# Kernel optimization log

Hardware: AMD Instinct MI355X
Metric: run time of the kernel (lower is better)

## Reference

```python
import jax, jax.numpy as jnp
import numpy as np

EMBED_DIM = 1024
NUM_HEADS = 16
HEAD_DIM = EMBED_DIM // NUM_HEADS


def setup_inputs() -> dict:
    key = jax.random.key(0)
    ks = jax.random.split(key, 5)
    scale = 1.0 / np.sqrt(EMBED_DIM)
    x = jax.random.normal(ks[0], (2, 2048, EMBED_DIM), dtype=jnp.float32)
    W_qkv = jax.random.uniform(ks[1], (EMBED_DIM, 3 * EMBED_DIM), jnp.float32, -scale, scale)
    b_qkv = jax.random.uniform(ks[2], (3 * EMBED_DIM,), jnp.float32, -scale, scale)
    W_out = jax.random.uniform(ks[3], (EMBED_DIM, EMBED_DIM), jnp.float32, -scale, scale)
    b_out = jax.random.uniform(ks[4], (EMBED_DIM,), jnp.float32, -scale, scale)
    return {"x": x, "W_qkv": W_qkv, "b_qkv": b_qkv, "W_out": W_out, "b_out": b_out}


def reference(x, W_qkv, b_qkv, W_out, b_out):
    B, T, C = x.shape
    H, D = NUM_HEADS, HEAD_DIM
    qkv = x @ W_qkv + b_qkv                       # [B,T,3C]
    q, k, v = jnp.split(qkv, 3, axis=-1)
    # [B,T,C] -> [B,H,T,D]
    q = q.reshape(B, T, H, D).transpose(0, 2, 1, 3)
    k = k.reshape(B, T, H, D).transpose(0, 2, 1, 3)
    v = v.reshape(B, T, H, D).transpose(0, 2, 1, 3)
    scores = jnp.einsum('bhqd,bhkd->bhqk', q, k) / np.sqrt(D)
    attn = jax.nn.softmax(scores, axis=-1)
    out = jnp.einsum('bhqk,bhkd->bhqd', attn, v)  # [B,H,T,D]
    out = out.transpose(0, 2, 1, 3).reshape(B, T, C)
    return out @ W_out + b_out
```

## Files before the change

kernel.cpp:

```cpp
#include <hip/hip_runtime.h>
#include <hip/hip_bf16.h>

#define TB 2048
#define CC 1024
#define HH 16
#define DD 64
#define MM 4096
#define N3 3072
#define KVB 128
#define NT (TB / KVB)

typedef __bf16 bf16x8 __attribute__((ext_vector_type(8)));
typedef float f32x4 __attribute__((ext_vector_type(4)));
typedef unsigned short ushort8 __attribute__((ext_vector_type(8)));
typedef unsigned short u16;

#define QSCALE 0.180336880693612f

__device__ __forceinline__ u16 f2b(float f) {
    unsigned int x = __float_as_uint(f);
    x = (x + 0x7fffu + ((x >> 16) & 1u)) >> 16;
    return (u16)x;
}

__device__ __forceinline__ unsigned cvt_pk_bf16(float lo, float hi) {
    unsigned r;
    asm("v_cvt_pk_bf16_f32 %0, %1, %2" : "=v"(r) : "v"(lo), "v"(hi));
    return r;
}

__device__ __forceinline__ void gld16(const u16* g, u16* l) {
    __builtin_amdgcn_global_load_lds(
        (const __attribute__((address_space(1))) unsigned int*)g,
        (__attribute__((address_space(3))) unsigned int*)l, 16, 0, 0);
}

__global__ __launch_bounds__(256) void prep(const float* __restrict__ x,
                                            u16* __restrict__ xb,
                                            const float* __restrict__ wqkv,
                                            u16* __restrict__ wqkvT,
                                            const float* __restrict__ wout,
                                            u16* __restrict__ woutT) {
    __shared__ float tl[64][65];
    const int bx = blockIdx.x;
    const int tid = threadIdx.x;
    if (bx < 4096) {
        int i = (bx * 256 + tid) * 4;
        float4 v = *reinterpret_cast<const float4*>(x + i);
        union { u16 u[4]; uint2 v2; } r;
        r.u[0] = f2b(v.x); r.u[1] = f2b(v.y); r.u[2] = f2b(v.z); r.u[3] = f2b(v.w);
        *reinterpret_cast<uint2*>(xb + i) = r.v2;
        return;
    }
    const int idx = bx - 4096;
    const int nb = idx & 63, kb = idx >> 6;
    const float* in; u16* out; int N, n0;
    if (nb < 48) { in = wqkv; out = wqkvT; N = 3072; n0 = nb * 64; }
    else         { in = wout; out = woutT; N = 1024; n0 = (nb - 48) * 64; }
    const int k0 = kb * 64;
#pragma unroll
    for (int rep = 0; rep < 16; ++rep) {
        int id2 = rep * 256 + tid;
        int r = id2 >> 6, c = id2 & 63;
        tl[r][c] = in[(size_t)(k0 + r) * N + n0 + c];
    }
    __syncthreads();
#pragma unroll
    for (int rep = 0; rep < 16; ++rep) {
        int id2 = rep * 256 + tid;
        int r = id2 >> 6, c = id2 & 63;
        out[(size_t)(n0 + r) * 1024 + k0 + c] = f2b(tl[c][r]);
    }
}

__global__ __launch_bounds__(256) void gemm_qkv(const u16* __restrict__ xb,
                                                const u16* __restrict__ wT,
                                                const float* __restrict__ bias,
                                                u16* __restrict__ qg,
                                                u16* __restrict__ kg,
                                                u16* __restrict__ vtg) {
    __shared__ u16 smem[2 * 128 * 64];
    u16* As = smem;
    u16* Bs = smem + 128 * 64;
    const int m0 = blockIdx.y * 128, n0 = blockIdx.x * 128;
    const int tid = threadIdx.x;
    const int w = tid >> 6, lane = tid & 63, lr = lane & 15, h = lane >> 4;
    const int wr = w >> 1, wc = w & 1;
    f32x4 acc[4][4] = {};

    for (int k0 = 0; k0 < 1024; k0 += 64) {
        __syncthreads();
#pragma unroll
        for (int j = 0; j < 4; ++j) {
            int L = j * 256 + tid;
            int r = L >> 3, c = L & 7;
            int csw = (c ^ (r & 7)) << 3;
            gld16(xb + (size_t)(m0 + r) * 1024 + k0 + csw, As + L * 8);
            gld16(wT + (size_t)(n0 + r) * 1024 + k0 + csw, Bs + L * 8);
        }
        __syncthreads();
#pragma unroll
        for (int kk = 0; kk < 2; ++kk) {
            bf16x8 a[4], b[4];
            int cc = kk * 4 + h;
#pragma unroll
            for (int m = 0; m < 4; ++m) {
                int R = wr * 64 + m * 16 + lr;
                a[m] = *reinterpret_cast<const bf16x8*>((const char*)As + R * 128 + ((cc ^ (R & 7)) << 4));
            }
#pragma unroll
            for (int n = 0; n < 4; ++n) {
                int R = wc * 64 + n * 16 + lr;
                b[n] = *reinterpret_cast<const bf16x8*>((const char*)Bs + R * 128 + ((cc ^ (R & 7)) << 4));
            }
#pragma unroll
            for (int m = 0; m < 4; ++m)
#pragma unroll
                for (int n = 0; n < 4; ++n)
                    acc[m][n] = __builtin_amdgcn_mfma_f32_16x16x32_bf16(a[m], b[n], acc[m][n], 0, 0, 0);
        }
    }

    const int nthird = n0 >> 10;
    const int b = m0 >> 11, t0 = m0 & 2047;
    if (nthird == 2) {
        __syncthreads();
#pragma unroll
        for (int n = 0; n < 4; ++n) {
            int nloc = wc * 64 + n * 16 + lr;
            unsigned xorv = (unsigned)(nloc & 15) << 4;
            float bv = bias[n0 + nloc];
#pragma unroll
            for (int m = 0; m < 4; ++m) {
                int mloc = wr * 64 + m * 16 + h * 4;
                int mp = (mloc & ~31) | (((mloc >> 2) & 3) << 3) | (((mloc >> 4) & 1) << 2);
                union { u16 u[4]; unsigned long long ll; } pk4;
#pragma unroll
                for (int reg = 0; reg < 4; ++reg)
                    pk4.u[reg] = f2b(acc[m][n][reg] + bv);
                *reinterpret_cast<unsigned long long*>(
                    (char*)smem + nloc * 256 + ((unsigned)(mp * 2) ^ xorv)) = pk4.ll;
            }
        }
        __syncthreads();
        const int c16 = tid & 15;
#pragma unroll
        for (int step = 0; step < 8; ++step) {
            int row = (tid >> 4) + step * 16;
            ushort8 vch = *reinterpret_cast<const ushort8*>(
                (const char*)smem + row * 256 + ((unsigned)((c16 ^ (row & 15)) << 4)));
            int c1 = (n0 + row) & 1023;
            int hh = c1 >> 6, dd = c1 & 63;
            *reinterpret_cast<ushort8*>(
                vtg + ((size_t)(b * HH + hh) * DD + dd) * TB + t0 + c16 * 8) = vch;
        }
    } else {
        const float qs = (nthird == 0) ? QSCALE : 1.0f;
        __syncthreads();
#pragma unroll
        for (int n = 0; n < 4; ++n) {
            int nloc = wc * 64 + n * 16 + lr;
            float bv = bias[n0 + nloc];
#pragma unroll
            for (int m = 0; m < 4; ++m) {
#pragma unroll
                for (int reg = 0; reg < 4; ++reg) {
                    int mloc = wr * 64 + m * 16 + h * 4 + reg;
                    *reinterpret_cast<u16*>((char*)smem + mloc * 256 +
                        ((unsigned)(nloc * 2) ^ ((unsigned)(mloc & 15) << 4)))
                        = f2b((acc[m][n][reg] + bv) * qs);
                }
            }
        }
        __syncthreads();
        u16* dst = (nthird == 0) ? qg : kg;
        const int c16 = tid & 15;
#pragma unroll
        for (int step = 0; step < 8; ++step) {
            int row = (tid >> 4) + step * 16;
            ushort8 vch = *reinterpret_cast<const ushort8*>(
                (const char*)smem + row * 256 + ((unsigned)((c16 ^ (row & 15)) << 4)));
            int colbase = c16 * 8;
            int c1 = (n0 + colbase) & 1023;
            int hh = c1 >> 6, dd = c1 & 63;
            *reinterpret_cast<ushort8*>(
                dst + ((size_t)(b * HH + hh) * TB + (t0 + row)) * DD + dd) = vch;
        }
    }
}

__global__ __launch_bounds__(512, 4) void attn(const u16* __restrict__ qg,
                                               const u16* __restrict__ kg,
                                               const u16* __restrict__ vtg,
                                               u16* __restrict__ ao) {
    __shared__ u16 Kt[2][KVB * 64];
    __shared__ u16 Vt[2][64 * KVB];
    const int bh = blockIdx.x;
    const int q0 = blockIdx.y * 128;
    const int tid = threadIdx.x, w = tid >> 6, lane = tid & 63;
    const int lr = lane & 15, h = lane >> 4;
    const u16* qb = qg + (size_t)bh * TB * DD;
    const u16* kb = kg + (size_t)bh * TB * DD;
    const u16* vb = vtg + (size_t)bh * DD * TB;

#define STAGE(buf, kp, vp) do {                                                         \
    _Pragma("unroll")                                                                   \
    for (int j = 0; j < 2; ++j) {                                                       \
        int L = j * 512 + tid;                                                          \
        int rk = L >> 3, ck = L & 7;                                                    \
        gld16((kp) + (size_t)rk * DD + ((ck ^ (rk & 7)) << 3), Kt[buf] + L * 8);        \
        int rv = L >> 4, cv = L & 15;                                                   \
        gld16((vp) + (size_t)rv * TB + ((cv ^ (rv & 15)) << 3), Vt[buf] + L * 8);       \
    } } while (0)

    bf16x8 bq[2];
#pragma unroll
    for (int kk = 0; kk < 2; ++kk)
        bq[kk] = *reinterpret_cast<const bf16x8*>(qb + (size_t)(q0 + w * 16 + lr) * DD + kk * 32 + h * 8);

    f32x4 o[4] = {};
    float m_r = -1e30f;
    float l_r = 0.f;
    const f32x4 zero4 = {0.f, 0.f, 0.f, 0.f};

    auto tile_body = [&](const u16* ktc, const u16* vtc) {
        f32x4 s[8];
        __builtin_amdgcn_s_setprio(1);
        {
            int cc0 = h;
#pragma unroll
            for (int ng = 0; ng < 8; ++ng) {
                int R = ng * 16 + lr;
                bf16x8 ak = *reinterpret_cast<const bf16x8*>((const char*)ktc + R * 128 + ((cc0 ^ (R & 7)) << 4));
                s[ng] = __builtin_amdgcn_mfma_f32_16x16x32_bf16(ak, bq[0], zero4, 0, 0, 0);
            }
            int cc1 = 4 + h;
#pragma unroll
            for (int ng = 0; ng < 8; ++ng) {
                int R = ng * 16 + lr;
                bf16x8 ak = *reinterpret_cast<const bf16x8*>((const char*)ktc + R * 128 + ((cc1 ^ (R & 7)) << 4));
                s[ng] = __builtin_amdgcn_mfma_f32_16x16x32_bf16(ak, bq[1], s[ng], 0, 0, 0);
            }
        }
        __builtin_amdgcn_s_setprio(0);

        float tmx[8];
#pragma unroll
        for (int ng = 0; ng < 8; ++ng)
            tmx[ng] = fmaxf(fmaxf(s[ng][0], s[ng][1]), fmaxf(s[ng][2], s[ng][3]));
        float pm = fmaxf(fmaxf(fmaxf(tmx[0], tmx[1]), fmaxf(tmx[2], tmx[3])),
                         fmaxf(fmaxf(tmx[4], tmx[5]), fmaxf(tmx[6], tmx[7])));
        pm = fmaxf(pm, __shfl_xor(pm, 16));
        pm = fmaxf(pm, __shfl_xor(pm, 32));

        if (!__all(pm - m_r <= 8.0f)) {
            float mn = fmaxf(m_r, pm);
            float fr = __builtin_amdgcn_exp2f(m_r - mn);
            m_r = mn;
            l_r *= fr;
#pragma unroll
            for (int reg = 0; reg < 4; ++reg) {
                float fro = __shfl(fr, h * 4 + reg);
#pragma unroll
                for (int ngd = 0; ngd < 4; ++ngd)
                    o[ngd][reg] *= fro;
            }
        }

        float ps[8];
#pragma unroll
        for (int ng = 0; ng < 8; ++ng) {
            s[ng][0] = __builtin_amdgcn_exp2f(s[ng][0] - m_r);
            s[ng][1] = __builtin_amdgcn_exp2f(s[ng][1] - m_r);
            s[ng][2] = __builtin_amdgcn_exp2f(s[ng][2] - m_r);
            s[ng][3] = __builtin_amdgcn_exp2f(s[ng][3] - m_r);
            ps[ng] = (s[ng][0] + s[ng][1]) + (s[ng][2] + s[ng][3]);
        }
        float sum = ((ps[0] + ps[1]) + (ps[2] + ps[3])) + ((ps[4] + ps[5]) + (ps[6] + ps[7]));
        sum += __shfl_xor(sum, 16);
        sum += __shfl_xor(sum, 32);
        l_r += sum;

        __builtin_amdgcn_s_setprio(1);
#pragma unroll
        for (int kk = 0; kk < 4; ++kk) {
            union { unsigned u[4]; bf16x8 v; } ap;
            ap.u[0] = cvt_pk_bf16(s[2 * kk][0], s[2 * kk][1]);
            ap.u[1] = cvt_pk_bf16(s[2 * kk][2], s[2 * kk][3]);
            ap.u[2] = cvt_pk_bf16(s[2 * kk + 1][0], s[2 * kk + 1][1]);
            ap.u[3] = cvt_pk_bf16(s[2 * kk + 1][2], s[2 * kk + 1][3]);
            int cpos = kk * 4 + h;
#pragma unroll
            for (int ngd = 0; ngd < 4; ++ngd) {
                int d = ngd * 16 + lr;
                bf16x8 bv = *reinterpret_cast<const bf16x8*>((const char*)vtc + d * 256 + ((cpos ^ (d & 15)) << 4));
                o[ngd] = __builtin_amdgcn_mfma_f32_16x16x32_bf16(ap.v, bv, o[ngd], 0, 0, 0);
            }
        }
        __builtin_amdgcn_s_setprio(0);
    };

    STAGE(0, kb, vb);
    const u16* kp = kb + KVB * DD;
    const u16* vp = vb + KVB;
    __syncthreads();

#pragma unroll 1
    for (int kt2 = 0; kt2 < NT / 2; ++kt2) {
        STAGE(1, kp, vp);
        kp += KVB * DD; vp += KVB;
        tile_body(Kt[0], Vt[0]);
        __syncthreads();
        if (kt2 < NT / 2 - 1) {
            STAGE(0, kp, vp);
            kp += KVB * DD; vp += KVB;
        }
        tile_body(Kt[1], Vt[1]);
        __syncthreads();
    }
#undef STAGE

    float linv[4];
#pragma unroll
    for (int reg = 0; reg < 4; ++reg)
        linv[reg] = 1.0f / __shfl(l_r, h * 4 + reg);

    const int b = bh >> 4, hh = bh & 15;
#pragma unroll
    for (int ngd = 0; ngd < 4; ++ngd) {
#pragma unroll
        for (int reg = 0; reg < 4; ++reg) {
            int t = q0 + w * 16 + h * 4 + reg;
            int col = hh * DD + ngd * 16 + lr;
            ao[((size_t)(b * TB + t)) * CC + col] = f2b(o[ngd][reg] * linv[reg]);
        }
    }
}

__global__ __launch_bounds__(256) void gemm_out(const u16* __restrict__ ao,
                                                const u16* __restrict__ wT,
                                                const float* __restrict__ bias,
                                                float* __restrict__ out) {
    __shared__ u16 As[64 * 64];
    __shared__ u16 Bs[128 * 64];
    const int m0 = blockIdx.y * 64, n0 = blockIdx.x * 128;
    const int tid = threadIdx.x;
    const int w = tid >> 6, lane = tid & 63, lr = lane & 15, h = lane >> 4;
    f32x4 acc[4][2] = {};

    for (int k0 = 0; k0 < 1024; k0 += 64) {
        __syncthreads();
#pragma unroll
        for (int j = 0; j < 2; ++j) {
            int L = j * 256 + tid;
            int r = L >> 3, c = L & 7;
            gld16(ao + (size_t)(m0 + r) * 1024 + k0 + ((c ^ (r & 7)) << 3), As + L * 8);
        }
#pragma unroll
        for (int j = 0; j < 4; ++j) {
            int L = j * 256 + tid;
            int r = L >> 3, c = L & 7;
            gld16(wT + (size_t)(n0 + r) * 1024 + k0 + ((c ^ (r & 7)) << 3), Bs + L * 8);
        }
        __syncthreads();
#pragma unroll
        for (int kk = 0; kk < 2; ++kk) {
            bf16x8 a[4], b[2];
            int cc = kk * 4 + h;
#pragma unroll
            for (int m = 0; m < 4; ++m) {
                int R = m * 16 + lr;
                a[m] = *reinterpret_cast<const bf16x8*>((const char*)As + R * 128 + ((cc ^ (R & 7)) << 4));
            }
#pragma unroll
            for (int n = 0; n < 2; ++n) {
                int R = w * 32 + n * 16 + lr;
                b[n] = *reinterpret_cast<const bf16x8*>((const char*)Bs + R * 128 + ((cc ^ (R & 7)) << 4));
            }
#pragma unroll
            for (int m = 0; m < 4; ++m)
#pragma unroll
                for (int n = 0; n < 2; ++n)
                    acc[m][n] = __builtin_amdgcn_mfma_f32_16x16x32_bf16(a[m], b[n], acc[m][n], 0, 0, 0);
        }
    }

#pragma unroll
    for (int n = 0; n < 2; ++n) {
        int ng = n0 + w * 32 + n * 16 + lr;
        float bv = bias[ng];
#pragma unroll
        for (int m = 0; m < 4; ++m) {
#pragma unroll
            for (int reg = 0; reg < 4; ++reg) {
                int mg = m0 + m * 16 + h * 4 + reg;
                out[(size_t)mg * 1024 + ng] = acc[m][n][reg] + bv;
            }
        }
    }
}

extern "C" void kernel_launch(void* const* d_in, const int* in_sizes, int n_in,
                              void* d_out, int out_size, void* d_ws, size_t ws_size,
                              hipStream_t stream) {
    const float* x     = (const float*)d_in[0];
    const float* W_qkv = (const float*)d_in[1];
    const float* b_qkv = (const float*)d_in[2];
    const float* W_out = (const float*)d_in[3];
    const float* b_out = (const float*)d_in[4];
    float* out = (float*)d_out;

    char* ws = (char*)d_ws;
    u16* xb    = (u16*)(ws);
    u16* wqkvT = (u16*)(ws + (size_t)( 8u << 20));
    u16* woutT = (u16*)(ws + (size_t)(14u << 20));
    u16* qg    = (u16*)(ws + (size_t)(16u << 20));
    u16* kg    = (u16*)(ws + (size_t)(24u << 20));
    u16* vtg   = (u16*)(ws + (size_t)(32u << 20));
    u16* ao    = xb;

    hipLaunchKernelGGL(prep, dim3(5120), dim3(256), 0, stream, x, xb, W_qkv, wqkvT, W_out, woutT);
    hipLaunchKernelGGL(gemm_qkv, dim3(24, 32), dim3(256), 0, stream, xb, wqkvT, b_qkv, qg, kg, vtg);
    hipLaunchKernelGGL(attn, dim3(32, 16), dim3(512), 0, stream, qg, kg, vtg, ao);
    hipLaunchKernelGGL(gemm_out, dim3(8, 64), dim3(256), 0, stream, ao, woutT, b_out, out);
}
```

Baseline: 118.4 us.

## Software-pipeline attention: overlap next tile's QK^T with current softmax and PV

```diff
diff --git a/kernel.cpp b/kernel.cpp
--- a/kernel.cpp
+++ b/kernel.cpp
@@ -203,15 +203,98 @@
     const u16* kb = kg + (size_t)bh * TB * DD;
     const u16* vb = vtg + (size_t)bh * DD * TB;
 
-#define STAGE(buf, kp, vp) do {                                                         \
+#define STAGE_K(buf, kt) do {                                                           \
     _Pragma("unroll")                                                                   \
     for (int j = 0; j < 2; ++j) {                                                       \
         int L = j * 512 + tid;                                                          \
         int rk = L >> 3, ck = L & 7;                                                    \
-        gld16((kp) + (size_t)rk * DD + ((ck ^ (rk & 7)) << 3), Kt[buf] + L * 8);        \
+        gld16(kb + (size_t)((kt) * KVB + rk) * DD + ((ck ^ (rk & 7)) << 3),             \
+              Kt[buf] + L * 8);                                                         \
+    } } while (0)
+#define STAGE_V(buf, kt) do {                                                           \
+    _Pragma("unroll")                                                                   \
+    for (int j = 0; j < 2; ++j) {                                                       \
+        int L = j * 512 + tid;                                                          \
         int rv = L >> 4, cv = L & 15;                                                   \
-        gld16((vp) + (size_t)rv * TB + ((cv ^ (rv & 15)) << 3), Vt[buf] + L * 8);       \
+        gld16(vb + (size_t)rv * TB + (kt) * KVB + ((cv ^ (rv & 15)) << 3),              \
+              Vt[buf] + L * 8);                                                         \
     } } while (0)
+
+#define QK_PHASE(S, KBUF) do {                                                          \
+    __builtin_amdgcn_s_setprio(1);                                                      \
+    const u16* ktc_ = Kt[KBUF];                                                         \
+    _Pragma("unroll")                                                                   \
+    for (int ng = 0; ng < 8; ++ng) {                                                    \
+        int R = ng * 16 + lr;                                                           \
+        bf16x8 ak = *reinterpret_cast<const bf16x8*>(                                   \
+            (const char*)ktc_ + R * 128 + (((h) ^ (R & 7)) << 4));                      \
+        S[ng] = __builtin_amdgcn_mfma_f32_16x16x32_bf16(ak, bq[0], zero4, 0, 0, 0);     \
+    }                                                                                   \
+    _Pragma("unroll")                                                                   \
+    for (int ng = 0; ng < 8; ++ng) {                                                    \
+        int R = ng * 16 + lr;                                                           \
+        bf16x8 ak = *reinterpret_cast<const bf16x8*>(                                   \
+            (const char*)ktc_ + R * 128 + (((4 + h) ^ (R & 7)) << 4));                  \
+        S[ng] = __builtin_amdgcn_mfma_f32_16x16x32_bf16(ak, bq[1], S[ng], 0, 0, 0);     \
+    }                                                                                   \
+    __builtin_amdgcn_s_setprio(0);                                                      \
+} while (0)
+
+#define SMPV(S, VBUF) do {                                                              \
+    const u16* vtc_ = Vt[VBUF];                                                         \
+    float tmx[8];                                                                       \
+    _Pragma("unroll")                                                                   \
+    for (int ng = 0; ng < 8; ++ng)                                                      \
+        tmx[ng] = fmaxf(fmaxf(S[ng][0], S[ng][1]), fmaxf(S[ng][2], S[ng][3]));          \
+    float pm = fmaxf(fmaxf(fmaxf(tmx[0], tmx[1]), fmaxf(tmx[2], tmx[3])),               \
+                     fmaxf(fmaxf(tmx[4], tmx[5]), fmaxf(tmx[6], tmx[7])));              \
+    pm = fmaxf(pm, __shfl_xor(pm, 16));                                                 \
+    pm = fmaxf(pm, __shfl_xor(pm, 32));                                                 \
+    if (!__all(pm - m_r <= 8.0f)) {                                                     \
+        float mn = fmaxf(m_r, pm);                                                      \
+        float fr = __builtin_amdgcn_exp2f(m_r - mn);                                    \
+        m_r = mn;                                                                       \
+        l_r *= fr;                                                                      \
+        _Pragma("unroll")                                                               \
+        for (int reg = 0; reg < 4; ++reg) {                                             \
+            float fro = __shfl(fr, h * 4 + reg);                                        \
+            _Pragma("unroll")                                                           \
+            for (int ngd = 0; ngd < 4; ++ngd)                                           \
+                o[ngd][reg] *= fro;                                                     \
+        }                                                                               \
+    }                                                                                   \
+    float ps[8];                                                                        \
+    _Pragma("unroll")                                                                   \
+    for (int ng = 0; ng < 8; ++ng) {                                                    \
+        S[ng][0] = __builtin_amdgcn_exp2f(S[ng][0] - m_r);                              \
+        S[ng][1] = __builtin_amdgcn_exp2f(S[ng][1] - m_r);                              \
+        S[ng][2] = __builtin_amdgcn_exp2f(S[ng][2] - m_r);                              \
+        S[ng][3] = __builtin_amdgcn_exp2f(S[ng][3] - m_r);                              \
+        ps[ng] = (S[ng][0] + S[ng][1]) + (S[ng][2] + S[ng][3]);                         \
+    }                                                                                   \
+    float sum = ((ps[0] + ps[1]) + (ps[2] + ps[3])) + ((ps[4] + ps[5]) + (ps[6] + ps[7])); \
+    sum += __shfl_xor(sum, 16);                                                         \
+    sum += __shfl_xor(sum, 32);                                                         \
+    l_r += sum;                                                                         \
+    __builtin_amdgcn_s_setprio(1);                                                      \
+    _Pragma("unroll")                                                                   \
+    for (int kk = 0; kk < 4; ++kk) {                                                    \
+        union { unsigned u[4]; bf16x8 v; } ap;                                          \
+        ap.u[0] = cvt_pk_bf16(S[2 * kk][0], S[2 * kk][1]);                              \
+        ap.u[1] = cvt_pk_bf16(S[2 * kk][2], S[2 * kk][3]);                              \
+        ap.u[2] = cvt_pk_bf16(S[2 * kk + 1][0], S[2 * kk + 1][1]);                      \
+        ap.u[3] = cvt_pk_bf16(S[2 * kk + 1][2], S[2 * kk + 1][3]);                      \
+        int cpos = kk * 4 + h;                                                          \
+        _Pragma("unroll")                                                               \
+        for (int ngd = 0; ngd < 4; ++ngd) {                                             \
+            int d = ngd * 16 + lr;                                                      \
+            bf16x8 bv = *reinterpret_cast<const bf16x8*>(                               \
+                (const char*)vtc_ + d * 256 + ((cpos ^ (d & 15)) << 4));                \
+            o[ngd] = __builtin_amdgcn_mfma_f32_16x16x32_bf16(ap.v, bv, o[ngd], 0, 0, 0);\
+        }                                                                               \
+    }                                                                                   \
+    __builtin_amdgcn_s_setprio(0);                                                      \
+} while (0)
 
     bf16x8 bq[2];
 #pragma unroll
@@ -222,103 +305,39 @@
     float m_r = -1e30f;
     float l_r = 0.f;
     const f32x4 zero4 = {0.f, 0.f, 0.f, 0.f};
-
-    auto tile_body = [&](const u16* ktc, const u16* vtc) {
-        f32x4 s[8];
-        __builtin_amdgcn_s_setprio(1);
-        {
-            int cc0 = h;
-#pragma unroll
-            for (int ng = 0; ng < 8; ++ng) {
-                int R = ng * 16 + lr;
-                bf16x8 ak = *reinterpret_cast<const bf16x8*>((const char*)ktc + R * 128 + ((cc0 ^ (R & 7)) << 4));
-                s[ng] = __builtin_amdgcn_mfma_f32_16x16x32_bf16(ak, bq[0], zero4, 0, 0, 0);
-            }
-            int cc1 = 4 + h;
-#pragma unroll
-            for (int ng = 0; ng < 8; ++ng) {
-                int R = ng * 16 + lr;
-                bf16x8 ak = *reinterpret_cast<const bf16x8*>((const char*)ktc + R * 128 + ((cc1 ^ (R & 7)) << 4));
-                s[ng] = __builtin_amdgcn_mfma_f32_16x16x32_bf16(ak, bq[1], s[ng], 0, 0, 0);
-            }
-        }
-        __builtin_amdgcn_s_setprio(0);
-
-        float tmx[8];
-#pragma unroll
-        for (int ng = 0; ng < 8; ++ng)
-            tmx[ng] = fmaxf(fmaxf(s[ng][0], s[ng][1]), fmaxf(s[ng][2], s[ng][3]));
-        float pm = fmaxf(fmaxf(fmaxf(tmx[0], tmx[1]), fmaxf(tmx[2], tmx[3])),
-                         fmaxf(fmaxf(tmx[4], tmx[5]), fmaxf(tmx[6], tmx[7])));
-        pm = fmaxf(pm, __shfl_xor(pm, 16));
-        pm = fmaxf(pm, __shfl_xor(pm, 32));
-
-        if (!__all(pm - m_r <= 8.0f)) {
-            float mn = fmaxf(m_r, pm);
-            float fr = __builtin_amdgcn_exp2f(m_r - mn);
-            m_r = mn;
-            l_r *= fr;
-#pragma unroll
-            for (int reg = 0; reg < 4; ++reg) {
-                float fro = __shfl(fr, h * 4 + reg);
-#pragma unroll
-                for (int ngd = 0; ngd < 4; ++ngd)
-                    o[ngd][reg] *= fro;
-            }
-        }
-
-        float ps[8];
-#pragma unroll
-        for (int ng = 0; ng < 8; ++ng) {
-            s[ng][0] = __builtin_amdgcn_exp2f(s[ng][0] - m_r);
-            s[ng][1] = __builtin_amdgcn_exp2f(s[ng][1] - m_r);
-            s[ng][2] = __builtin_amdgcn_exp2f(s[ng][2] - m_r);
-            s[ng][3] = __builtin_amdgcn_exp2f(s[ng][3] - m_r);
-            ps[ng] = (s[ng][0] + s[ng][1]) + (s[ng][2] + s[ng][3]);
-        }
-        float sum = ((ps[0] + ps[1]) + (ps[2] + ps[3])) + ((ps[4] + ps[5]) + (ps[6] + ps[7]));
-        sum += __shfl_xor(sum, 16);
-        sum += __shfl_xor(sum, 32);
-        l_r += sum;
-
-        __builtin_amdgcn_s_setprio(1);
-#pragma unroll
-        for (int kk = 0; kk < 4; ++kk) {
-            union { unsigned u[4]; bf16x8 v; } ap;
-            ap.u[0] = cvt_pk_bf16(s[2 * kk][0], s[2 * kk][1]);
-            ap.u[1] = cvt_pk_bf16(s[2 * kk][2], s[2 * kk][3]);
-            ap.u[2] = cvt_pk_bf16(s[2 * kk + 1][0], s[2 * kk + 1][1]);
-            ap.u[3] = cvt_pk_bf16(s[2 * kk + 1][2], s[2 * kk + 1][3]);
-            int cpos = kk * 4 + h;
-#pragma unroll
-            for (int ngd = 0; ngd < 4; ++ngd) {
-                int d = ngd * 16 + lr;
-                bf16x8 bv = *reinterpret_cast<const bf16x8*>((const char*)vtc + d * 256 + ((cpos ^ (d & 15)) << 4));
-                o[ngd] = __builtin_amdgcn_mfma_f32_16x16x32_bf16(ap.v, bv, o[ngd], 0, 0, 0);
-            }
-        }
-        __builtin_amdgcn_s_setprio(0);
-    };
-
-    STAGE(0, kb, vb);
-    const u16* kp = kb + KVB * DD;
-    const u16* vp = vb + KVB;
+    f32x4 sA[8], sB[8];
+
+    STAGE_K(0, 0);
+    STAGE_V(0, 0);
+    STAGE_K(1, 1);
     __syncthreads();
+    QK_PHASE(sA, 0);
+    __syncthreads();
 
 #pragma unroll 1
-    for (int kt2 = 0; kt2 < NT / 2; ++kt2) {
-        STAGE(1, kp, vp);
-        kp += KVB * DD; vp += KVB;
-        tile_body(Kt[0], Vt[0]);
-        __syncthreads();
-        if (kt2 < NT / 2 - 1) {
-            STAGE(0, kp, vp);
-            kp += KVB * DD; vp += KVB;
-        }
-        tile_body(Kt[1], Vt[1]);
-        __syncthreads();
-    }
-#undef STAGE
+    for (int u = 0; u < 7; ++u) {
+        const int t = 2 * u;
+        STAGE_V(1, t + 1);
+        STAGE_K(0, t + 2);
+        QK_PHASE(sB, 1);
+        SMPV(sA, 0);
+        __syncthreads();
+        STAGE_V(0, t + 2);
+        STAGE_K(1, t + 3);
+        QK_PHASE(sA, 0);
+        SMPV(sB, 1);
+        __syncthreads();
+    }
+    STAGE_V(1, 15);
+    QK_PHASE(sB, 1);
+    SMPV(sA, 0);
+    __syncthreads();
+    SMPV(sB, 1);
+
+#undef STAGE_K
+#undef STAGE_V
+#undef QK_PHASE
+#undef SMPV
 
     float linv[4];
 #pragma unroll
```

After: 129.1 us. 1.09x slower.

## Switch attention to 32x32x16 MFMA with 4 waves of 32 query rows

Applied to the files above, without the earlier changes.

```diff
diff --git a/kernel.cpp b/kernel.cpp
--- a/kernel.cpp
+++ b/kernel.cpp
@@ -12,6 +12,7 @@
 
 typedef __bf16 bf16x8 __attribute__((ext_vector_type(8)));
 typedef float f32x4 __attribute__((ext_vector_type(4)));
+typedef float f32x16 __attribute__((ext_vector_type(16)));
 typedef unsigned short ushort8 __attribute__((ext_vector_type(8)));
 typedef unsigned short u16;
 
@@ -133,7 +134,7 @@
 #pragma unroll
             for (int m = 0; m < 4; ++m) {
                 int mloc = wr * 64 + m * 16 + h * 4;
-                int mp = (mloc & ~31) | (((mloc >> 2) & 3) << 3) | (((mloc >> 4) & 1) << 2);
+                int mp = (mloc & ~15) | (mloc & 3) | ((mloc & 4) << 1) | ((mloc & 8) >> 1);
                 union { u16 u[4]; unsigned long long ll; } pk4;
 #pragma unroll
                 for (int reg = 0; reg < 4; ++reg)
@@ -189,7 +190,7 @@
     }
 }
 
-__global__ __launch_bounds__(512, 4) void attn(const u16* __restrict__ qg,
+__global__ __launch_bounds__(256, 2) void attn(const u16* __restrict__ qg,
                                                const u16* __restrict__ kg,
                                                const u16* __restrict__ vtg,
                                                u16* __restrict__ ao) {
@@ -198,59 +199,58 @@
     const int bh = blockIdx.x;
     const int q0 = blockIdx.y * 128;
     const int tid = threadIdx.x, w = tid >> 6, lane = tid & 63;
-    const int lr = lane & 15, h = lane >> 4;
+    const int ln = lane & 31, H = lane >> 5;
     const u16* qb = qg + (size_t)bh * TB * DD;
     const u16* kb = kg + (size_t)bh * TB * DD;
     const u16* vb = vtg + (size_t)bh * DD * TB;
 
 #define STAGE(buf, kp, vp) do {                                                         \
     _Pragma("unroll")                                                                   \
-    for (int j = 0; j < 2; ++j) {                                                       \
-        int L = j * 512 + tid;                                                          \
+    for (int j = 0; j < 4; ++j) {                                                       \
+        int L = j * 256 + tid;                                                          \
         int rk = L >> 3, ck = L & 7;                                                    \
         gld16((kp) + (size_t)rk * DD + ((ck ^ (rk & 7)) << 3), Kt[buf] + L * 8);        \
         int rv = L >> 4, cv = L & 15;                                                   \
         gld16((vp) + (size_t)rv * TB + ((cv ^ (rv & 15)) << 3), Vt[buf] + L * 8);       \
     } } while (0)
 
-    bf16x8 bq[2];
-#pragma unroll
-    for (int kk = 0; kk < 2; ++kk)
-        bq[kk] = *reinterpret_cast<const bf16x8*>(qb + (size_t)(q0 + w * 16 + lr) * DD + kk * 32 + h * 8);
-
-    f32x4 o[4] = {};
+    bf16x8 bq[4];
+#pragma unroll
+    for (int dc = 0; dc < 4; ++dc)
+        bq[dc] = *reinterpret_cast<const bf16x8*>(
+            qb + (size_t)(q0 + w * 32 + ln) * DD + dc * 16 + H * 8);
+
+    f32x16 o[2] = {};
     float m_r = -1e30f;
     float l_r = 0.f;
-    const f32x4 zero4 = {0.f, 0.f, 0.f, 0.f};
+    f32x16 zero16 = {};
 
     auto tile_body = [&](const u16* ktc, const u16* vtc) {
-        f32x4 s[8];
+        f32x16 s[4];
         __builtin_amdgcn_s_setprio(1);
-        {
-            int cc0 = h;
-#pragma unroll
-            for (int ng = 0; ng < 8; ++ng) {
-                int R = ng * 16 + lr;
-                bf16x8 ak = *reinterpret_cast<const bf16x8*>((const char*)ktc + R * 128 + ((cc0 ^ (R & 7)) << 4));
-                s[ng] = __builtin_amdgcn_mfma_f32_16x16x32_bf16(ak, bq[0], zero4, 0, 0, 0);
-            }
-            int cc1 = 4 + h;
-#pragma unroll
-            for (int ng = 0; ng < 8; ++ng) {
-                int R = ng * 16 + lr;
-                bf16x8 ak = *reinterpret_cast<const bf16x8*>((const char*)ktc + R * 128 + ((cc1 ^ (R & 7)) << 4));
-                s[ng] = __builtin_amdgcn_mfma_f32_16x16x32_bf16(ak, bq[1], s[ng], 0, 0, 0);
+#pragma unroll
+        for (int kb4 = 0; kb4 < 4; ++kb4) {
+            int R = kb4 * 32 + ln;
+            const char* krow = (const char*)ktc + R * 128;
+#pragma unroll
+            for (int dc = 0; dc < 4; ++dc) {
+                bf16x8 ak = *reinterpret_cast<const bf16x8*>(
+                    krow + (((dc * 2 + H) ^ (R & 7)) << 4));
+                s[kb4] = __builtin_amdgcn_mfma_f32_32x32x16_bf16(
+                    ak, bq[dc], dc == 0 ? zero16 : s[kb4], 0, 0, 0);
             }
         }
         __builtin_amdgcn_s_setprio(0);
 
-        float tmx[8];
-#pragma unroll
-        for (int ng = 0; ng < 8; ++ng)
-            tmx[ng] = fmaxf(fmaxf(s[ng][0], s[ng][1]), fmaxf(s[ng][2], s[ng][3]));
-        float pm = fmaxf(fmaxf(fmaxf(tmx[0], tmx[1]), fmaxf(tmx[2], tmx[3])),
-                         fmaxf(fmaxf(tmx[4], tmx[5]), fmaxf(tmx[6], tmx[7])));
-        pm = fmaxf(pm, __shfl_xor(pm, 16));
+        float pm = s[0][0];
+#pragma unroll
+        for (int kb4 = 0; kb4 < 4; ++kb4) {
+            float t0 = fmaxf(fmaxf(s[kb4][0], s[kb4][1]), fmaxf(s[kb4][2], s[kb4][3]));
+            float t1 = fmaxf(fmaxf(s[kb4][4], s[kb4][5]), fmaxf(s[kb4][6], s[kb4][7]));
+            float t2 = fmaxf(fmaxf(s[kb4][8], s[kb4][9]), fmaxf(s[kb4][10], s[kb4][11]));
+            float t3 = fmaxf(fmaxf(s[kb4][12], s[kb4][13]), fmaxf(s[kb4][14], s[kb4][15]));
+            pm = fmaxf(pm, fmaxf(fmaxf(t0, t1), fmaxf(t2, t3)));
+        }
         pm = fmaxf(pm, __shfl_xor(pm, 32));
 
         if (!__all(pm - m_r <= 8.0f)) {
@@ -259,42 +259,44 @@
             m_r = mn;
             l_r *= fr;
 #pragma unroll
-            for (int reg = 0; reg < 4; ++reg) {
-                float fro = __shfl(fr, h * 4 + reg);
-#pragma unroll
-                for (int ngd = 0; ngd < 4; ++ngd)
-                    o[ngd][reg] *= fro;
-            }
-        }
-
-        float ps[8];
-#pragma unroll
-        for (int ng = 0; ng < 8; ++ng) {
-            s[ng][0] = __builtin_amdgcn_exp2f(s[ng][0] - m_r);
-            s[ng][1] = __builtin_amdgcn_exp2f(s[ng][1] - m_r);
-            s[ng][2] = __builtin_amdgcn_exp2f(s[ng][2] - m_r);
-            s[ng][3] = __builtin_amdgcn_exp2f(s[ng][3] - m_r);
-            ps[ng] = (s[ng][0] + s[ng][1]) + (s[ng][2] + s[ng][3]);
-        }
-        float sum = ((ps[0] + ps[1]) + (ps[2] + ps[3])) + ((ps[4] + ps[5]) + (ps[6] + ps[7]));
-        sum += __shfl_xor(sum, 16);
+            for (int ngd = 0; ngd < 2; ++ngd)
+#pragma unroll
+                for (int r = 0; r < 16; ++r)
+                    o[ngd][r] *= fr;
+        }
+
+        float sum = 0.f;
+#pragma unroll
+        for (int kb4 = 0; kb4 < 4; ++kb4) {
+            float ps = 0.f;
+#pragma unroll
+            for (int r = 0; r < 16; ++r) {
+                s[kb4][r] = __builtin_amdgcn_exp2f(s[kb4][r] - m_r);
+                ps += s[kb4][r];
+            }
+            sum += ps;
+        }
         sum += __shfl_xor(sum, 32);
         l_r += sum;
 
         __builtin_amdgcn_s_setprio(1);
 #pragma unroll
-        for (int kk = 0; kk < 4; ++kk) {
-            union { unsigned u[4]; bf16x8 v; } ap;
-            ap.u[0] = cvt_pk_bf16(s[2 * kk][0], s[2 * kk][1]);
-            ap.u[1] = cvt_pk_bf16(s[2 * kk][2], s[2 * kk][3]);
-            ap.u[2] = cvt_pk_bf16(s[2 * kk + 1][0], s[2 * kk + 1][1]);
-            ap.u[3] = cvt_pk_bf16(s[2 * kk + 1][2], s[2 * kk + 1][3]);
-            int cpos = kk * 4 + h;
-#pragma unroll
-            for (int ngd = 0; ngd < 4; ++ngd) {
-                int d = ngd * 16 + lr;
-                bf16x8 bv = *reinterpret_cast<const bf16x8*>((const char*)vtc + d * 256 + ((cpos ^ (d & 15)) << 4));
-                o[ngd] = __builtin_amdgcn_mfma_f32_16x16x32_bf16(ap.v, bv, o[ngd], 0, 0, 0);
+        for (int kb4 = 0; kb4 < 4; ++kb4) {
+#pragma unroll
+            for (int b1 = 0; b1 < 2; ++b1) {
+                union { unsigned u[4]; bf16x8 v; } ap;
+                ap.u[0] = cvt_pk_bf16(s[kb4][8 * b1 + 0], s[kb4][8 * b1 + 1]);
+                ap.u[1] = cvt_pk_bf16(s[kb4][8 * b1 + 2], s[kb4][8 * b1 + 3]);
+                ap.u[2] = cvt_pk_bf16(s[kb4][8 * b1 + 4], s[kb4][8 * b1 + 5]);
+                ap.u[3] = cvt_pk_bf16(s[kb4][8 * b1 + 6], s[kb4][8 * b1 + 7]);
+                int c = kb4 * 2 + b1;
+#pragma unroll
+                for (int ngd = 0; ngd < 2; ++ngd) {
+                    int d = ngd * 32 + ln;
+                    bf16x8 av = *reinterpret_cast<const bf16x8*>(
+                        (const char*)vtc + d * 256 + (((c * 2 + H) ^ (d & 15)) << 4));
+                    o[ngd] = __builtin_amdgcn_mfma_f32_32x32x16_bf16(av, ap.v, o[ngd], 0, 0, 0);
+                }
             }
         }
         __builtin_amdgcn_s_setprio(0);
@@ -320,19 +322,20 @@
     }
 #undef STAGE
 
-    float linv[4];
-#pragma unroll
-    for (int reg = 0; reg < 4; ++reg)
-        linv[reg] = 1.0f / __shfl(l_r, h * 4 + reg);
-
+    const float linv = 1.0f / l_r;
     const int b = bh >> 4, hh = bh & 15;
-#pragma unroll
-    for (int ngd = 0; ngd < 4; ++ngd) {
-#pragma unroll
-        for (int reg = 0; reg < 4; ++reg) {
-            int t = q0 + w * 16 + h * 4 + reg;
-            int col = hh * DD + ngd * 16 + lr;
-            ao[((size_t)(b * TB + t)) * CC + col] = f2b(o[ngd][reg] * linv[reg]);
+    const int q = q0 + w * 32 + ln;
+    u16* aorow = ao + (size_t)(b * TB + q) * CC + hh * 64;
+#pragma unroll
+    for (int ngd = 0; ngd < 2; ++ngd) {
+#pragma unroll
+        for (int rg = 0; rg < 4; ++rg) {
+            int dbase = ngd * 32 + 8 * rg + 4 * H;
+            union { u16 u[4]; unsigned long long ll; } pk;
+#pragma unroll
+            for (int r2 = 0; r2 < 4; ++r2)
+                pk.u[r2] = f2b(o[ngd][4 * rg + r2] * linv);
+            *reinterpret_cast<unsigned long long*>(aorow + dbase) = pk.ll;
         }
     }
 }
@@ -421,6 +424,6 @@
 
     hipLaunchKernelGGL(prep, dim3(5120), dim3(256), 0, stream, x, xb, W_qkv, wqkvT, W_out, woutT);
     hipLaunchKernelGGL(gemm_qkv, dim3(24, 32), dim3(256), 0, stream, xb, wqkvT, b_qkv, qg, kg, vtg);
-    hipLaunchKernelGGL(attn, dim3(32, 16), dim3(512), 0, stream, qg, kg, vtg, ao);
+    hipLaunchKernelGGL(attn, dim3(32, 16), dim3(256), 0, stream, qg, kg, vtg, ao);
     hipLaunchKernelGGL(gemm_out, dim3(8, 64), dim3(256), 0, stream, ao, woutT, b_out, out);
 }
```

Measured after the change: 118.7 us. About the same (+0.3%).
